# Performance work log

Measured on AMD Instinct MI355X. Metric: run time of the kernel, lower is better.

## Reference

```python
import jax, jax.numpy as jnp
import numpy as np

B, N, C, H = 8, 1024, 768, 12
D = C // H          # head_dim = 64
M = 2 * D           # rand_feat_dim = 128
SCALE = D ** -0.5
EPS = 1e-12         # F.normalize eps


def _feature_map(z, rand_matrix):
    # z: [B,H,N,D] already multiplied by sqrt(scale); proj: [H,D,M]
    logits = jnp.einsum('bhnd,hdm->bhnm', z, rand_matrix)
    sqnorm = 0.5 * jnp.sum(z * z, axis=-1, keepdims=True)
    return jnp.exp(logits - sqnorm) * (M ** -0.5)


def setup_inputs() -> dict:
    key = jax.random.key(0)
    k1, k2, k3, k4, k5 = jax.random.split(key, 5)
    x = jax.random.normal(k1, (B, N, C), dtype=jnp.float32)
    qkv_w = jax.random.normal(k2, (3 * C, C), dtype=jnp.float32) * 0.02
    proj_w = jax.random.normal(k3, (C, C), dtype=jnp.float32) * 0.02
    proj_b = jax.random.normal(k4, (C,), dtype=jnp.float32) * 0.02
    rand_matrix = jax.random.normal(k5, (H, D, M), dtype=jnp.float32)
    return {"x": x, "qkv_w": qkv_w, "proj_w": proj_w, "proj_b": proj_b,
            "rand_matrix": rand_matrix}


def reference(x, qkv_w, proj_w, proj_b, rand_matrix):
    b, n, c = x.shape
    # qkv projection (torch Linear, no bias): [B,N,3C] -> [3,B,H,N,D]
    qkv = (x @ qkv_w.T).reshape(b, n, 3, H, D).transpose(2, 0, 3, 1, 4)
    q, k, v = qkv[0], qkv[1], qkv[2]
    sq = SCALE ** 0.5
    qf = _feature_map(q * sq, rand_matrix)   # [B,H,N,M]
    kf = _feature_map(k * sq, rand_matrix)   # [B,H,N,M]
    attn = jnp.einsum('bhnm,bhkm->bhnk', qf, kf)          # explicit O(N^2)
    denom = jnp.maximum(jnp.sum(jnp.abs(attn), axis=-1, keepdims=True), EPS)
    attn = attn / denom                                   # L1 normalize
    out = jnp.einsum('bhnk,bhkd->bhnd', attn, v)          # [B,H,N,D]
    out = out.transpose(0, 2, 1, 3).reshape(b, n, c)
    return out @ proj_w.T + proj_b
```

## Files before the change

### kernel.cpp

```cpp
#include <hip/hip_runtime.h>
#include <hip/hip_bf16.h>

#define PB 8
#define PN 1024
#define PC 768
#define PH 12
#define PD 64
#define PM 128
#define SQ 0.35355339059327373f
#define MSCALE 0.08838834764831843f

typedef _Float16 f16;
typedef f16 f16x8 __attribute__((ext_vector_type(8)));
typedef f16 f16x4 __attribute__((ext_vector_type(4)));
typedef float f32x4 __attribute__((ext_vector_type(4)));

__global__ __launch_bounds__(192) void conv_hi(const float* __restrict__ src,
                                               f16* __restrict__ dst, int cols) {
    const int r = blockIdx.x;
    const int c = threadIdx.x * 4;
    float4 v = *(const float4*)&src[(size_t)r * cols + c];
    f16x4 hi;
    hi.x = (f16)v.x; hi.y = (f16)v.y; hi.z = (f16)v.z; hi.w = (f16)v.w;
    *(f16x4*)&dst[(size_t)r * cols + c] = hi;
}

__global__ __launch_bounds__(256) void conv_rt(const float* __restrict__ rm,
                                               f16* __restrict__ Rt) {
    const int h = blockIdx.x;
    for (int e = threadIdx.x; e < PD * PM; e += 256) {
        int m = e >> 6, d = e & 63;
        Rt[(size_t)h * PD * PM + e] = (f16)rm[(size_t)h * PD * PM + d * PM + m];
    }
}

__global__ __launch_bounds__(256) void gemm_qkv(
        const f16* __restrict__ A,
        const f16* __restrict__ Bm,
        f16* __restrict__ zq, f16* __restrict__ zk, f16* __restrict__ vh,
        float* __restrict__ sqq, float* __restrict__ sqk)
{
    __shared__ f16 As[128 * 32];
    __shared__ f16 Bs[128 * 32];
    const int t = threadIdx.x;
    const int wave = t >> 6, lane = t & 63;
    const int wm = wave >> 1, wn = wave & 1;
    const int bi = blockIdx.y * 128, bj = blockIdx.x * 128;

    f32x4 acc[4][4] = {};

    const int srow16 = lane >> 2;
    const int schunk = ((lane & 3) ^ ((lane >> 3) & 3)) * 8;
    const f16* Ap = A + (size_t)(bi + wave * 32 + srow16) * PC + schunk;
    f16* AsB = &As[wave * 32 * 32];
    const f16* Bp = Bm + (size_t)(bj + wave * 32 + srow16) * PC + schunk;
    f16* BsB = &Bs[wave * 32 * 32];

    for (int kt = 0; kt < 24; ++kt) {
        const int k0 = kt * 32;
        __syncthreads();
        __builtin_amdgcn_global_load_lds(
            (const __attribute__((address_space(1))) void*)(Ap + k0),
            (__attribute__((address_space(3))) void*)(AsB), 16, 0, 0);
        __builtin_amdgcn_global_load_lds(
            (const __attribute__((address_space(1))) void*)(Ap + k0 + (size_t)16 * PC),
            (__attribute__((address_space(3))) void*)(AsB + 16 * 32), 16, 0, 0);
        __builtin_amdgcn_global_load_lds(
            (const __attribute__((address_space(1))) void*)(Bp + k0),
            (__attribute__((address_space(3))) void*)(BsB), 16, 0, 0);
        __builtin_amdgcn_global_load_lds(
            (const __attribute__((address_space(1))) void*)(Bp + k0 + (size_t)16 * PC),
            (__attribute__((address_space(3))) void*)(BsB + 16 * 32), 16, 0, 0);
        __syncthreads();

        f16x8 af[4], bf[4];
        #pragma unroll
        for (int i = 0; i < 4; ++i) {
            const int r = wm * 64 + i * 16 + (lane & 15);
            const int p = (lane >> 4) ^ ((r >> 1) & 3);
            af[i] = *(const f16x8*)&As[r * 32 + p * 8];
        }
        #pragma unroll
        for (int j = 0; j < 4; ++j) {
            const int r = wn * 64 + j * 16 + (lane & 15);
            const int p = (lane >> 4) ^ ((r >> 1) & 3);
            bf[j] = *(const f16x8*)&Bs[r * 32 + p * 8];
        }
        #pragma unroll
        for (int i = 0; i < 4; ++i)
            #pragma unroll
            for (int j = 0; j < 4; ++j)
                acc[i][j] = __builtin_amdgcn_mfma_f32_16x16x32_f16(af[i], bf[j], acc[i][j], 0, 0, 0);
    }

    const int quad = lane >> 4, cc = lane & 15;
    const int colbase = bj + wn * 64;
    const int b = bi >> 10;
    if (colbase < 1536) {
        const int which = colbase >= 768;
        const int h = (colbase - which * 768) >> 6;
        f16* zdst = which ? zk : zq;
        float* sdst = which ? sqk : sqq;
        const size_t bh = (size_t)(b * PH + h);
        #pragma unroll
        for (int i = 0; i < 4; ++i) {
            const int row0 = bi + wm * 64 + i * 16 + quad * 4;
            #pragma unroll
            for (int r = 0; r < 4; ++r) {
                const int n = (row0 + r) & 1023;
                f16 zh[4]; float psq = 0.f;
                #pragma unroll
                for (int j = 0; j < 4; ++j) {
                    zh[j] = (f16)(acc[i][j][r] * SQ);
                    float zf = (float)zh[j];
                    psq += zf * zf;
                }
                psq += __shfl_xor(psq, 1, 64);
                psq += __shfl_xor(psq, 2, 64);
                psq += __shfl_xor(psq, 4, 64);
                psq += __shfl_xor(psq, 8, 64);
                if (cc == 0) sdst[(bh << 10) + n] = 0.5f * psq;
                f16* zp = zdst + (((bh << 10) + n) << 6);
                #pragma unroll
                for (int j = 0; j < 4; ++j) zp[j * 16 + cc] = zh[j];
            }
        }
    } else {
        const int h = (colbase - 1536) >> 6;
        const size_t bh = (size_t)(b * PH + h);
        #pragma unroll
        for (int i = 0; i < 4; ++i) {
            const int row0 = bi + wm * 64 + i * 16 + quad * 4;
            #pragma unroll
            for (int r = 0; r < 4; ++r) {
                const int n = (row0 + r) & 1023;
                f16* vp = vh + (((bh << 10) + n) << 6);
                #pragma unroll
                for (int j = 0; j < 4; ++j) vp[j * 16 + cc] = (f16)acc[i][j][r];
            }
        }
    }
}

__global__ __launch_bounds__(256) void feat_kv(
        const f16* __restrict__ zk, const f16* __restrict__ Rt,
        const float* __restrict__ sqk, const f16* __restrict__ vh,
        float* __restrict__ kvp, float* __restrict__ sbufp)
{
    __shared__ __align__(16) char smem[52224];
    f16* As = (f16*)smem;
    f16* Bs = (f16*)(smem + 8192);
    f16* Pt = (f16*)smem;
    f16* vT = (f16*)(smem + 34816);
    __shared__ float sqs[128];

    const int t = threadIdx.x;
    const int wave = t >> 6, lane = t & 63;
    const int wm = wave >> 1, wn = wave & 1;
    const int nt = blockIdx.x, bh = blockIdx.y;
    const int h = bh % PH;

    const f16* A = zk + (((size_t)bh << 10) + nt * 128) * 64;
    const f16* Bm = Rt + (size_t)h * (PM * PD);

    if (t < 128) sqs[t] = sqk[((size_t)bh << 10) + nt * 128 + t];

    f32x4 acc[4][4] = {};
    const int srow16 = lane >> 2;
    const int schunk = ((lane & 3) ^ ((lane >> 3) & 3)) * 8;
    const f16* Ap = A + (size_t)(wave * 32 + srow16) * 64 + schunk;
    f16* AsB = &As[wave * 32 * 32];
    const f16* Bp = Bm + (size_t)(wave * 32 + srow16) * 64 + schunk;
    f16* BsB = &Bs[wave * 32 * 32];

    #pragma unroll
    for (int kt = 0; kt < 2; ++kt) {
        const int k0 = kt * 32;
        __syncthreads();
        __builtin_amdgcn_global_load_lds(
            (const __attribute__((address_space(1))) void*)(Ap + k0),
            (__attribute__((address_space(3))) void*)(AsB), 16, 0, 0);
        __builtin_amdgcn_global_load_lds(
            (const __attribute__((address_space(1))) void*)(Ap + k0 + (size_t)16 * 64),
            (__attribute__((address_space(3))) void*)(AsB + 16 * 32), 16, 0, 0);
        __builtin_amdgcn_global_load_lds(
            (const __attribute__((address_space(1))) void*)(Bp + k0),
            (__attribute__((address_space(3))) void*)(BsB), 16, 0, 0);
        __builtin_amdgcn_global_load_lds(
            (const __attribute__((address_space(1))) void*)(Bp + k0 + (size_t)16 * 64),
            (__attribute__((address_space(3))) void*)(BsB + 16 * 32), 16, 0, 0);
        __syncthreads();

        f16x8 af[4], bf[4];
        #pragma unroll
        for (int i = 0; i < 4; ++i) {
            const int r = wm * 64 + i * 16 + (lane & 15);
            const int p = (lane >> 4) ^ ((r >> 1) & 3);
            af[i] = *(const f16x8*)&As[r * 32 + p * 8];
        }
        #pragma unroll
        for (int j = 0; j < 4; ++j) {
            const int r = wn * 64 + j * 16 + (lane & 15);
            const int p = (lane >> 4) ^ ((r >> 1) & 3);
            bf[j] = *(const f16x8*)&Bs[r * 32 + p * 8];
        }
        #pragma unroll
        for (int i = 0; i < 4; ++i)
            #pragma unroll
            for (int j = 0; j < 4; ++j)
                acc[i][j] = __builtin_amdgcn_mfma_f32_16x16x32_f16(af[i], bf[j], acc[i][j], 0, 0, 0);
    }

    const int quad = lane >> 4, cc = lane & 15;
    __syncthreads();

    #pragma unroll
    for (int i = 0; i < 4; ++i) {
        #pragma unroll
        for (int j = 0; j < 4; ++j) {
            const int col = wn * 64 + j * 16 + cc;
            #pragma unroll
            for (int r = 0; r < 4; ++r) {
                const int rl = wm * 64 + i * 16 + quad * 4 + r;
                Pt[col * 136 + rl] = (f16)(__expf(acc[i][j][r] - sqs[rl]) * MSCALE);
            }
        }
    }
    {
        const int vn = t >> 1;
        const int vhf = (t & 1) * 32;
        const f16* vbase = vh + (((size_t)bh << 10) + nt * 128 + vn) * 64 + vhf;
        #pragma unroll
        for (int k = 0; k < 4; ++k) {
            f16x8 vv = *(const f16x8*)&vbase[k * 8];
            #pragma unroll
            for (int e = 0; e < 8; ++e)
                vT[(vhf + k * 8 + e) * 136 + vn] = vv[e];
        }
    }
    __syncthreads();

    f32x4 acc2[4][2] = {};
    #pragma unroll
    for (int kt = 0; kt < 4; ++kt) {
        const int kb = kt * 32 + (lane >> 4) * 8;
        f16x8 af2[4], bf2[2];
        #pragma unroll
        for (int i = 0; i < 4; ++i)
            af2[i] = *(const f16x8*)&Pt[(wm * 64 + i * 16 + (lane & 15)) * 136 + kb];
        #pragma unroll
        for (int j = 0; j < 2; ++j)
            bf2[j] = *(const f16x8*)&vT[(wn * 32 + j * 16 + (lane & 15)) * 136 + kb];
        #pragma unroll
        for (int i = 0; i < 4; ++i)
            #pragma unroll
            for (int j = 0; j < 2; ++j)
                acc2[i][j] = __builtin_amdgcn_mfma_f32_16x16x32_f16(af2[i], bf2[j], acc2[i][j], 0, 0, 0);
    }

    float* kvo = kvp + (size_t)(nt * 96 + bh) * 8192;
    #pragma unroll
    for (int i = 0; i < 4; ++i) {
        #pragma unroll
        for (int j = 0; j < 2; ++j) {
            const int d = wn * 32 + j * 16 + cc;
            #pragma unroll
            for (int r = 0; r < 4; ++r) {
                const int m = wm * 64 + i * 16 + quad * 4 + r;
                kvo[m * 64 + d] = acc2[i][j][r];
            }
        }
    }
    {
        const int sm = t >> 1, shf = (t & 1) * 64;
        float sp = 0.f;
        #pragma unroll
        for (int k = 0; k < 8; ++k) {
            f16x8 pv = *(const f16x8*)&Pt[sm * 136 + shf + k * 8];
            #pragma unroll
            for (int e = 0; e < 8; ++e) sp += (float)pv[e];
        }
        sp += __shfl_xor(sp, 1, 64);
        if ((t & 1) == 0) sbufp[(size_t)(nt * 96 + bh) * 128 + sm] = sp;
    }
}

__global__ __launch_bounds__(256) void kv_reduce(
        const float* __restrict__ kvp, const float* __restrict__ sbufp,
        float* __restrict__ kv, float* __restrict__ s)
{
    const int idx = blockIdx.x * 256 + threadIdx.x;
    float a = 0.f;
    #pragma unroll
    for (int c = 0; c < 8; ++c) a += kvp[(size_t)c * 786432 + idx];
    kv[idx] = a;
    if (idx < 96 * PM) {
        float sa = 0.f;
        #pragma unroll
        for (int c = 0; c < 8; ++c) sa += sbufp[(size_t)c * 96 * PM + idx];
        s[idx] = sa;
    }
}

__global__ __launch_bounds__(256) void feat_apply(
        const f16* __restrict__ zq, const f16* __restrict__ Rt,
        const float* __restrict__ sqq, const float* __restrict__ kvf,
        const float* __restrict__ sf, f16* __restrict__ ohA)
{
    __shared__ __align__(16) char smem[52224];
    f16* As = (f16*)smem;
    f16* Bs = (f16*)(smem + 8192);
    f16* Pn = (f16*)smem;
    f16* kvT = (f16*)(smem + 34816);
    __shared__ float sqs[128], ssm[128], dns[128];

    const int t = threadIdx.x;
    const int wave = t >> 6, lane = t & 63;
    const int wm = wave >> 1, wn = wave & 1;
    const int nt = blockIdx.x, bh = blockIdx.y;
    const int b = bh / PH, h = bh % PH;

    const f16* A = zq + (((size_t)bh << 10) + nt * 128) * 64;
    const f16* Bm = Rt + (size_t)h * (PM * PD);

    if (t < 128) {
        sqs[t] = sqq[((size_t)bh << 10) + nt * 128 + t];
        ssm[t] = sf[(size_t)bh * 128 + t];
    }

    f32x4 acc[4][4] = {};
    const int srow16 = lane >> 2;
    const int schunk = ((lane & 3) ^ ((lane >> 3) & 3)) * 8;
    const f16* Ap = A + (size_t)(wave * 32 + srow16) * 64 + schunk;
    f16* AsB = &As[wave * 32 * 32];
    const f16* Bp = Bm + (size_t)(wave * 32 + srow16) * 64 + schunk;
    f16* BsB = &Bs[wave * 32 * 32];

    #pragma unroll
    for (int kt = 0; kt < 2; ++kt) {
        const int k0 = kt * 32;
        __syncthreads();
        __builtin_amdgcn_global_load_lds(
            (const __attribute__((address_space(1))) void*)(Ap + k0),
            (__attribute__((address_space(3))) void*)(AsB), 16, 0, 0);
        __builtin_amdgcn_global_load_lds(
            (const __attribute__((address_space(1))) void*)(Ap + k0 + (size_t)16 * 64),
            (__attribute__((address_space(3))) void*)(AsB + 16 * 32), 16, 0, 0);
        __builtin_amdgcn_global_load_lds(
            (const __attribute__((address_space(1))) void*)(Bp + k0),
            (__attribute__((address_space(3))) void*)(BsB), 16, 0, 0);
        __builtin_amdgcn_global_load_lds(
            (const __attribute__((address_space(1))) void*)(Bp + k0 + (size_t)16 * 64),
            (__attribute__((address_space(3))) void*)(BsB + 16 * 32), 16, 0, 0);
        __syncthreads();

        f16x8 af[4], bf[4];
        #pragma unroll
        for (int i = 0; i < 4; ++i) {
            const int r = wm * 64 + i * 16 + (lane & 15);
            const int p = (lane >> 4) ^ ((r >> 1) & 3);
            af[i] = *(const f16x8*)&As[r * 32 + p * 8];
        }
        #pragma unroll
        for (int j = 0; j < 4; ++j) {
            const int r = wn * 64 + j * 16 + (lane & 15);
            const int p = (lane >> 4) ^ ((r >> 1) & 3);
            bf[j] = *(const f16x8*)&Bs[r * 32 + p * 8];
        }
        #pragma unroll
        for (int i = 0; i < 4; ++i)
            #pragma unroll
            for (int j = 0; j < 4; ++j)
                acc[i][j] = __builtin_amdgcn_mfma_f32_16x16x32_f16(af[i], bf[j], acc[i][j], 0, 0, 0);
    }

    const int quad = lane >> 4, cc = lane & 15;
    __syncthreads();

    #pragma unroll
    for (int i = 0; i < 4; ++i) {
        #pragma unroll
        for (int j = 0; j < 4; ++j) {
            const int col = wn * 64 + j * 16 + cc;
            #pragma unroll
            for (int r = 0; r < 4; ++r) {
                const int rl = wm * 64 + i * 16 + quad * 4 + r;
                Pn[rl * 136 + col] = (f16)(__expf(acc[i][j][r] - sqs[rl]) * MSCALE);
            }
        }
    }
    {
        const int m = t >> 1;
        const int dh2 = (t & 1) * 32;
        const float* kvb = kvf + ((size_t)bh * 128 + m) * 64 + dh2;
        #pragma unroll
        for (int k = 0; k < 8; ++k) {
            float4 k4 = *(const float4*)&kvb[k * 4];
            kvT[(dh2 + k * 4 + 0) * 136 + m] = (f16)k4.x;
            kvT[(dh2 + k * 4 + 1) * 136 + m] = (f16)k4.y;
            kvT[(dh2 + k * 4 + 2) * 136 + m] = (f16)k4.z;
            kvT[(dh2 + k * 4 + 3) * 136 + m] = (f16)k4.w;
        }
    }
    __syncthreads();

    {
        const int n = t >> 1, mh = (t & 1) * 64;
        float p = 0.f;
        #pragma unroll
        for (int k = 0; k < 8; ++k) {
            f16x8 pv = *(const f16x8*)&Pn[n * 136 + mh + k * 8];
            #pragma unroll
            for (int e = 0; e < 8; ++e)
                p += (float)pv[e] * ssm[mh + k * 8 + e];
        }
        p += __shfl_xor(p, 1, 64);
        if ((t & 1) == 0) dns[n] = (p < 1e-12f) ? 1e-12f : p;
    }
    __syncthreads();

    f32x4 acc3[4][2] = {};
    #pragma unroll
    for (int kt = 0; kt < 4; ++kt) {
        const int kb = kt * 32 + (lane >> 4) * 8;
        f16x8 af3[4], bf3[2];
        #pragma unroll
        for (int i = 0; i < 4; ++i)
            af3[i] = *(const f16x8*)&Pn[(wm * 64 + i * 16 + (lane & 15)) * 136 + kb];
        #pragma unroll
        for (int j = 0; j < 2; ++j)
            bf3[j] = *(const f16x8*)&kvT[(wn * 32 + j * 16 + (lane & 15)) * 136 + kb];
        #pragma unroll
        for (int i = 0; i < 4; ++i)
            #pragma unroll
            for (int j = 0; j < 2; ++j)
                acc3[i][j] = __builtin_amdgcn_mfma_f32_16x16x32_f16(af3[i], bf3[j], acc3[i][j], 0, 0, 0);
    }

    f16* ob = ohA + ((size_t)(b * PN) + nt * 128) * PC + h * PD;
    #pragma unroll
    for (int i = 0; i < 4; ++i) {
        #pragma unroll
        for (int j = 0; j < 2; ++j) {
            const int d = wn * 32 + j * 16 + cc;
            #pragma unroll
            for (int r = 0; r < 4; ++r) {
                const int n = wm * 64 + i * 16 + quad * 4 + r;
                ob[(size_t)n * PC + d] = (f16)(acc3[i][j][r] / dns[n]);
            }
        }
    }
}

template<int BN>
__global__ __launch_bounds__(256) void gemm_mfma(
        const f16* __restrict__ A, int lda,
        const f16* __restrict__ Bm, int ldb,
        float* __restrict__ Cm, int ldc, int Kp,
        const float* __restrict__ bias)
{
    constexpr int JT = BN / 32;
    __shared__ f16 As[128 * 32];
    __shared__ f16 Bs[BN * 32];
    const int t = threadIdx.x;
    const int wave = t >> 6, lane = t & 63;
    const int wm = wave >> 1, wn = wave & 1;
    const int bi = blockIdx.y * 128, bj = blockIdx.x * BN;

    f32x4 acc[4][JT] = {};

    const int srow16 = lane >> 2;
    const int schunk = ((lane & 3) ^ ((lane >> 3) & 3)) * 8;
    const f16* Ap = A + (size_t)(bi + wave * 32 + srow16) * lda + schunk;
    f16* AsB = &As[wave * 32 * 32];
    const int brow0 = (BN == 128) ? wave * 32 : wave * 16;
    const f16* Bp = Bm + (size_t)(bj + brow0 + srow16) * ldb + schunk;
    f16* BsB = &Bs[brow0 * 32];

    const int nK = Kp / 32;
    for (int kt = 0; kt < nK; ++kt) {
        const int k0 = kt * 32;
        __syncthreads();
        __builtin_amdgcn_global_load_lds(
            (const __attribute__((address_space(1))) void*)(Ap + k0),
            (__attribute__((address_space(3))) void*)(AsB), 16, 0, 0);
        __builtin_amdgcn_global_load_lds(
            (const __attribute__((address_space(1))) void*)(Ap + k0 + (size_t)16 * lda),
            (__attribute__((address_space(3))) void*)(AsB + 16 * 32), 16, 0, 0);
        __builtin_amdgcn_global_load_lds(
            (const __attribute__((address_space(1))) void*)(Bp + k0),
            (__attribute__((address_space(3))) void*)(BsB), 16, 0, 0);
        if (BN == 128)
            __builtin_amdgcn_global_load_lds(
                (const __attribute__((address_space(1))) void*)(Bp + k0 + (size_t)16 * ldb),
                (__attribute__((address_space(3))) void*)(BsB + 16 * 32), 16, 0, 0);
        __syncthreads();

        f16x8 af[4], bf[JT];
        #pragma unroll
        for (int i = 0; i < 4; ++i) {
            const int r = wm * 64 + i * 16 + (lane & 15);
            const int p = (lane >> 4) ^ ((r >> 1) & 3);
            af[i] = *(const f16x8*)&As[r * 32 + p * 8];
        }
        #pragma unroll
        for (int j = 0; j < JT; ++j) {
            const int r = wn * (BN / 2) + j * 16 + (lane & 15);
            const int p = (lane >> 4) ^ ((r >> 1) & 3);
            bf[j] = *(const f16x8*)&Bs[r * 32 + p * 8];
        }
        #pragma unroll
        for (int i = 0; i < 4; ++i)
            #pragma unroll
            for (int j = 0; j < JT; ++j)
                acc[i][j] = __builtin_amdgcn_mfma_f32_16x16x32_f16(af[i], bf[j], acc[i][j], 0, 0, 0);
    }

    const int cr = (lane >> 4) * 4, cc = lane & 15;
    #pragma unroll
    for (int i = 0; i < 4; ++i) {
        const int row = bi + wm * 64 + i * 16 + cr;
        #pragma unroll
        for (int j = 0; j < JT; ++j) {
            const int col = bj + wn * (BN / 2) + j * 16 + cc;
            const float bv = bias ? bias[col] : 0.f;
            #pragma unroll
            for (int r = 0; r < 4; ++r)
                Cm[(size_t)(row + r) * ldc + col] = acc[i][j][r] + bv;
        }
    }
}

extern "C" void kernel_launch(void* const* d_in, const int* in_sizes, int n_in,
                              void* d_out, int out_size, void* d_ws, size_t ws_size,
                              hipStream_t stream) {
    const float* x      = (const float*)d_in[0];
    const float* qkv_w  = (const float*)d_in[1];
    const float* proj_w = (const float*)d_in[2];
    const float* proj_b = (const float*)d_in[3];
    const float* rm     = (const float*)d_in[4];
    float* out = (float*)d_out;

    char* ws = (char*)d_ws;
    f16*   Ax   = (f16*)(ws);
    f16*   Bqk  = (f16*)(ws + 12582912);
    f16*   Bp   = (f16*)(ws + 16121856);
    f16*   Rt   = (f16*)(ws + 17301504);
    f16*   zq   = (f16*)(ws + 17498112);
    f16*   zk   = (f16*)(ws + 30081024);
    f16*   vh   = (f16*)(ws + 42663936);
    float* sqq  = (float*)(ws + 55246848);
    float* sqk  = (float*)(ws + 55640064);
    float* sbufp= (float*)(ws + 56033280);
    float* kvf  = (float*)(ws + 56426496);
    float* sf   = (float*)(ws + 59572224);
    f16*   ohA  = (f16*)(ws + 59621376);
    float* kvp = (float*)d_out;

    conv_hi<<<8192, 192, 0, stream>>>(x, Ax, PC);
    conv_hi<<<2304, 192, 0, stream>>>(qkv_w, Bqk, PC);
    conv_hi<<<768, 192, 0, stream>>>(proj_w, Bp, PC);
    conv_rt<<<PH, 256, 0, stream>>>(rm, Rt);

    gemm_qkv<<<dim3(18, 64), 256, 0, stream>>>(Ax, Bqk, zq, zk, vh, sqq, sqk);

    feat_kv<<<dim3(8, 96), 256, 0, stream>>>(zk, Rt, sqk, vh, kvp, sbufp);
    kv_reduce<<<3072, 256, 0, stream>>>(kvp, sbufp, kvf, sf);

    feat_apply<<<dim3(8, 96), 256, 0, stream>>>(zq, Rt, sqq, kvf, sf, ohA);

    gemm_mfma<64><<<dim3(12, 64), 256, 0, stream>>>(ohA, PC, Bp, PC,
                                                    out, PC, PC, proj_b);
}
```

Measured before the change: 202.3 us.

## Widen GEMM K-tile to 64 with 8-way swizzle and fuse conversion kernels

Doubles the K-depth of the shared-memory tiles in the QKV, feature and projection GEMMs from 32 to 64, using a new 8-chunk XOR swizzle. This halves the number of barrier pairs per K loop and loads each feature kernel's operands in a single pass. It also merges the four fp32-to-fp16 conversion launches into one kernel, saving launch overhead. The cost is twice the LDS per GEMM block, which may lower occupancy, and more complex swizzled addressing that must stay bank-conflict free.

Measured after the change: 189.5 us. 1.07x faster.

```diff
diff --git a/kernel.cpp b/kernel.cpp
--- a/kernel.cpp
+++ b/kernel.cpp
@@ -15,22 +15,32 @@
 typedef f16 f16x4 __attribute__((ext_vector_type(4)));
 typedef float f32x4 __attribute__((ext_vector_type(4)));
 
-__global__ __launch_bounds__(192) void conv_hi(const float* __restrict__ src,
-                                               f16* __restrict__ dst, int cols) {
-    const int r = blockIdx.x;
-    const int c = threadIdx.x * 4;
-    float4 v = *(const float4*)&src[(size_t)r * cols + c];
-    f16x4 hi;
-    hi.x = (f16)v.x; hi.y = (f16)v.y; hi.z = (f16)v.z; hi.w = (f16)v.w;
-    *(f16x4*)&dst[(size_t)r * cols + c] = hi;
-}
-
-__global__ __launch_bounds__(256) void conv_rt(const float* __restrict__ rm,
-                                               f16* __restrict__ Rt) {
-    const int h = blockIdx.x;
-    for (int e = threadIdx.x; e < PD * PM; e += 256) {
-        int m = e >> 6, d = e & 63;
-        Rt[(size_t)h * PD * PM + e] = (f16)rm[(size_t)h * PD * PM + d * PM + m];
+#define GLL(src, dst) __builtin_amdgcn_global_load_lds( \
+    (const __attribute__((address_space(1))) void*)(src), \
+    (__attribute__((address_space(3))) void*)(dst), 16, 0, 0)
+
+__global__ __launch_bounds__(192) void conv_all(
+        const float* __restrict__ x, const float* __restrict__ qkv_w,
+        const float* __restrict__ proj_w, const float* __restrict__ rm,
+        f16* __restrict__ Ax, f16* __restrict__ Bqk, f16* __restrict__ Bp,
+        f16* __restrict__ Rt)
+{
+    const int bid = blockIdx.x;
+    const int t = threadIdx.x;
+    if (bid < 11264) {
+        const float* src; f16* dst; int r;
+        if (bid < 8192)       { src = x;      dst = Ax;  r = bid; }
+        else if (bid < 10496) { src = qkv_w;  dst = Bqk; r = bid - 8192; }
+        else                  { src = proj_w; dst = Bp;  r = bid - 10496; }
+        const int c = t * 4;
+        float4 v = *(const float4*)&src[(size_t)r * PC + c];
+        f16x4 hv;
+        hv.x = (f16)v.x; hv.y = (f16)v.y; hv.z = (f16)v.z; hv.w = (f16)v.w;
+        *(f16x4*)&dst[(size_t)r * PC + c] = hv;
+    } else {
+        const int h = bid - 11264;
+        for (int e = t; e < PD * PM; e += 192)
+            Rt[(size_t)h * 8192 + e] = (f16)rm[(size_t)h * 8192 + (e & 63) * PM + (e >> 6)];
     }
 }
 
@@ -40,8 +50,8 @@
         f16* __restrict__ zq, f16* __restrict__ zk, f16* __restrict__ vh,
         float* __restrict__ sqq, float* __restrict__ sqk)
 {
-    __shared__ f16 As[128 * 32];
-    __shared__ f16 Bs[128 * 32];
+    __shared__ f16 As[128 * 64];
+    __shared__ f16 Bs[128 * 64];
     const int t = threadIdx.x;
     const int wave = t >> 6, lane = t & 63;
     const int wm = wave >> 1, wn = wave & 1;
@@ -49,48 +59,50 @@
 
     f32x4 acc[4][4] = {};
 
-    const int srow16 = lane >> 2;
-    const int schunk = ((lane & 3) ^ ((lane >> 3) & 3)) * 8;
-    const f16* Ap = A + (size_t)(bi + wave * 32 + srow16) * PC + schunk;
-    f16* AsB = &As[wave * 32 * 32];
-    const f16* Bp = Bm + (size_t)(bj + wave * 32 + srow16) * PC + schunk;
-    f16* BsB = &Bs[wave * 32 * 32];
-
-    for (int kt = 0; kt < 24; ++kt) {
-        const int k0 = kt * 32;
+    const int rowi = lane >> 3;
+    const int cb = (lane & 7) ^ ((lane >> 4) & 3);
+    const f16* ApE = A + (size_t)(bi + wave * 32 + rowi) * PC + cb * 8;
+    const f16* ApO = A + (size_t)(bi + wave * 32 + rowi) * PC + (cb ^ 4) * 8;
+    const f16* BpE = Bm + (size_t)(bj + wave * 32 + rowi) * PC + cb * 8;
+    const f16* BpO = Bm + (size_t)(bj + wave * 32 + rowi) * PC + (cb ^ 4) * 8;
+    f16* AsB = &As[wave * 32 * 64];
+    f16* BsB = &Bs[wave * 32 * 64];
+
+    const int q4 = lane >> 4;
+    for (int kt = 0; kt < 12; ++kt) {
+        const int k0 = kt * 64;
         __syncthreads();
-        __builtin_amdgcn_global_load_lds(
-            (const __attribute__((address_space(1))) void*)(Ap + k0),
-            (__attribute__((address_space(3))) void*)(AsB), 16, 0, 0);
-        __builtin_amdgcn_global_load_lds(
-            (const __attribute__((address_space(1))) void*)(Ap + k0 + (size_t)16 * PC),
-            (__attribute__((address_space(3))) void*)(AsB + 16 * 32), 16, 0, 0);
-        __builtin_amdgcn_global_load_lds(
-            (const __attribute__((address_space(1))) void*)(Bp + k0),
-            (__attribute__((address_space(3))) void*)(BsB), 16, 0, 0);
-        __builtin_amdgcn_global_load_lds(
-            (const __attribute__((address_space(1))) void*)(Bp + k0 + (size_t)16 * PC),
-            (__attribute__((address_space(3))) void*)(BsB + 16 * 32), 16, 0, 0);
+        GLL(ApE + k0,               AsB);
+        GLL(ApO + k0 + (size_t) 8 * PC, AsB + 8 * 64);
+        GLL(ApE + k0 + (size_t)16 * PC, AsB + 16 * 64);
+        GLL(ApO + k0 + (size_t)24 * PC, AsB + 24 * 64);
+        GLL(BpE + k0,               BsB);
+        GLL(BpO + k0 + (size_t) 8 * PC, BsB + 8 * 64);
+        GLL(BpE + k0 + (size_t)16 * PC, BsB + 16 * 64);
+        GLL(BpO + k0 + (size_t)24 * PC, BsB + 24 * 64);
         __syncthreads();
 
-        f16x8 af[4], bf[4];
-        #pragma unroll
-        for (int i = 0; i < 4; ++i) {
-            const int r = wm * 64 + i * 16 + (lane & 15);
-            const int p = (lane >> 4) ^ ((r >> 1) & 3);
-            af[i] = *(const f16x8*)&As[r * 32 + p * 8];
-        }
-        #pragma unroll
-        for (int j = 0; j < 4; ++j) {
-            const int r = wn * 64 + j * 16 + (lane & 15);
-            const int p = (lane >> 4) ^ ((r >> 1) & 3);
-            bf[j] = *(const f16x8*)&Bs[r * 32 + p * 8];
-        }
-        #pragma unroll
-        for (int i = 0; i < 4; ++i)
-            #pragma unroll
-            for (int j = 0; j < 4; ++j)
-                acc[i][j] = __builtin_amdgcn_mfma_f32_16x16x32_f16(af[i], bf[j], acc[i][j], 0, 0, 0);
+        #pragma unroll
+        for (int kh = 0; kh < 2; ++kh) {
+            f16x8 af[4], bf[4];
+            #pragma unroll
+            for (int i = 0; i < 4; ++i) {
+                const int r = wm * 64 + i * 16 + (lane & 15);
+                const int p = (kh * 4 + q4) ^ ((r >> 1) & 7);
+                af[i] = *(const f16x8*)&As[r * 64 + p * 8];
+            }
+            #pragma unroll
+            for (int j = 0; j < 4; ++j) {
+                const int r = wn * 64 + j * 16 + (lane & 15);
+                const int p = (kh * 4 + q4) ^ ((r >> 1) & 7);
+                bf[j] = *(const f16x8*)&Bs[r * 64 + p * 8];
+            }
+            #pragma unroll
+            for (int i = 0; i < 4; ++i)
+                #pragma unroll
+                for (int j = 0; j < 4; ++j)
+                    acc[i][j] = __builtin_amdgcn_mfma_f32_16x16x32_f16(af[i], bf[j], acc[i][j], 0, 0, 0);
+        }
     }
 
     const int quad = lane >> 4, cc = lane & 15;
@@ -149,7 +161,7 @@
 {
     __shared__ __align__(16) char smem[52224];
     f16* As = (f16*)smem;
-    f16* Bs = (f16*)(smem + 8192);
+    f16* Bs = (f16*)(smem + 16384);
     f16* Pt = (f16*)smem;
     f16* vT = (f16*)(smem + 34816);
     __shared__ float sqs[128];
@@ -165,44 +177,40 @@
 
     if (t < 128) sqs[t] = sqk[((size_t)bh << 10) + nt * 128 + t];
 
+    const int rowi = lane >> 3;
+    const int cb = (lane & 7) ^ ((lane >> 4) & 3);
+    const f16* ApE = A + (size_t)(wave * 32 + rowi) * 64 + cb * 8;
+    const f16* ApO = A + (size_t)(wave * 32 + rowi) * 64 + (cb ^ 4) * 8;
+    const f16* BpE = Bm + (size_t)(wave * 32 + rowi) * 64 + cb * 8;
+    const f16* BpO = Bm + (size_t)(wave * 32 + rowi) * 64 + (cb ^ 4) * 8;
+    f16* AsB = &As[wave * 32 * 64];
+    f16* BsB = &Bs[wave * 32 * 64];
+    GLL(ApE,            AsB);
+    GLL(ApO + 8 * 64,   AsB + 8 * 64);
+    GLL(ApE + 16 * 64,  AsB + 16 * 64);
+    GLL(ApO + 24 * 64,  AsB + 24 * 64);
+    GLL(BpE,            BsB);
+    GLL(BpO + 8 * 64,   BsB + 8 * 64);
+    GLL(BpE + 16 * 64,  BsB + 16 * 64);
+    GLL(BpO + 24 * 64,  BsB + 24 * 64);
+    __syncthreads();
+
+    const int q4 = lane >> 4;
     f32x4 acc[4][4] = {};
-    const int srow16 = lane >> 2;
-    const int schunk = ((lane & 3) ^ ((lane >> 3) & 3)) * 8;
-    const f16* Ap = A + (size_t)(wave * 32 + srow16) * 64 + schunk;
-    f16* AsB = &As[wave * 32 * 32];
-    const f16* Bp = Bm + (size_t)(wave * 32 + srow16) * 64 + schunk;
-    f16* BsB = &Bs[wave * 32 * 32];
-
-    #pragma unroll
-    for (int kt = 0; kt < 2; ++kt) {
-        const int k0 = kt * 32;
-        __syncthreads();
-        __builtin_amdgcn_global_load_lds(
-            (const __attribute__((address_space(1))) void*)(Ap + k0),
-            (__attribute__((address_space(3))) void*)(AsB), 16, 0, 0);
-        __builtin_amdgcn_global_load_lds(
-            (const __attribute__((address_space(1))) void*)(Ap + k0 + (size_t)16 * 64),
-            (__attribute__((address_space(3))) void*)(AsB + 16 * 32), 16, 0, 0);
-        __builtin_amdgcn_global_load_lds(
-            (const __attribute__((address_space(1))) void*)(Bp + k0),
-            (__attribute__((address_space(3))) void*)(BsB), 16, 0, 0);
-        __builtin_amdgcn_global_load_lds(
-            (const __attribute__((address_space(1))) void*)(Bp + k0 + (size_t)16 * 64),
-            (__attribute__((address_space(3))) void*)(BsB + 16 * 32), 16, 0, 0);
-        __syncthreads();
-
+    #pragma unroll
+    for (int kh = 0; kh < 2; ++kh) {
         f16x8 af[4], bf[4];
         #pragma unroll
         for (int i = 0; i < 4; ++i) {
             const int r = wm * 64 + i * 16 + (lane & 15);
-            const int p = (lane >> 4) ^ ((r >> 1) & 3);
-            af[i] = *(const f16x8*)&As[r * 32 + p * 8];
+            const int p = (kh * 4 + q4) ^ ((r >> 1) & 7);
+            af[i] = *(const f16x8*)&As[r * 64 + p * 8];
         }
         #pragma unroll
         for (int j = 0; j < 4; ++j) {
             const int r = wn * 64 + j * 16 + (lane & 15);
-            const int p = (lane >> 4) ^ ((r >> 1) & 3);
-            bf[j] = *(const f16x8*)&Bs[r * 32 + p * 8];
+            const int p = (kh * 4 + q4) ^ ((r >> 1) & 7);
+            bf[j] = *(const f16x8*)&Bs[r * 64 + p * 8];
         }
         #pragma unroll
         for (int i = 0; i < 4; ++i)
@@ -309,7 +317,7 @@
 {
     __shared__ __align__(16) char smem[52224];
     f16* As = (f16*)smem;
-    f16* Bs = (f16*)(smem + 8192);
+    f16* Bs = (f16*)(smem + 16384);
     f16* Pn = (f16*)smem;
     f16* kvT = (f16*)(smem + 34816);
     __shared__ float sqs[128], ssm[128], dns[128];
@@ -328,44 +336,40 @@
         ssm[t] = sf[(size_t)bh * 128 + t];
     }
 
+    const int rowi = lane >> 3;
+    const int cb = (lane & 7) ^ ((lane >> 4) & 3);
+    const f16* ApE = A + (size_t)(wave * 32 + rowi) * 64 + cb * 8;
+    const f16* ApO = A + (size_t)(wave * 32 + rowi) * 64 + (cb ^ 4) * 8;
+    const f16* BpE = Bm + (size_t)(wave * 32 + rowi) * 64 + cb * 8;
+    const f16* BpO = Bm + (size_t)(wave * 32 + rowi) * 64 + (cb ^ 4) * 8;
+    f16* AsB = &As[wave * 32 * 64];
+    f16* BsB = &Bs[wave * 32 * 64];
+    GLL(ApE,            AsB);
+    GLL(ApO + 8 * 64,   AsB + 8 * 64);
+    GLL(ApE + 16 * 64,  AsB + 16 * 64);
+    GLL(ApO + 24 * 64,  AsB + 24 * 64);
+    GLL(BpE,            BsB);
+    GLL(BpO + 8 * 64,   BsB + 8 * 64);
+    GLL(BpE + 16 * 64,  BsB + 16 * 64);
+    GLL(BpO + 24 * 64,  BsB + 24 * 64);
+    __syncthreads();
+
+    const int q4 = lane >> 4;
     f32x4 acc[4][4] = {};
-    const int srow16 = lane >> 2;
-    const int schunk = ((lane & 3) ^ ((lane >> 3) & 3)) * 8;
-    const f16* Ap = A + (size_t)(wave * 32 + srow16) * 64 + schunk;
-    f16* AsB = &As[wave * 32 * 32];
-    const f16* Bp = Bm + (size_t)(wave * 32 + srow16) * 64 + schunk;
-    f16* BsB = &Bs[wave * 32 * 32];
-
-    #pragma unroll
-    for (int kt = 0; kt < 2; ++kt) {
-        const int k0 = kt * 32;
-        __syncthreads();
-        __builtin_amdgcn_global_load_lds(
-            (const __attribute__((address_space(1))) void*)(Ap + k0),
-            (__attribute__((address_space(3))) void*)(AsB), 16, 0, 0);
-        __builtin_amdgcn_global_load_lds(
-            (const __attribute__((address_space(1))) void*)(Ap + k0 + (size_t)16 * 64),
-            (__attribute__((address_space(3))) void*)(AsB + 16 * 32), 16, 0, 0);
-        __builtin_amdgcn_global_load_lds(
-            (const __attribute__((address_space(1))) void*)(Bp + k0),
-            (__attribute__((address_space(3))) void*)(BsB), 16, 0, 0);
-        __builtin_amdgcn_global_load_lds(
-            (const __attribute__((address_space(1))) void*)(Bp + k0 + (size_t)16 * 64),
-            (__attribute__((address_space(3))) void*)(BsB + 16 * 32), 16, 0, 0);
-        __syncthreads();
-
+    #pragma unroll
+    for (int kh = 0; kh < 2; ++kh) {
         f16x8 af[4], bf[4];
         #pragma unroll
         for (int i = 0; i < 4; ++i) {
             const int r = wm * 64 + i * 16 + (lane & 15);
-            const int p = (lane >> 4) ^ ((r >> 1) & 3);
-            af[i] = *(const f16x8*)&As[r * 32 + p * 8];
+            const int p = (kh * 4 + q4) ^ ((r >> 1) & 7);
+            af[i] = *(const f16x8*)&As[r * 64 + p * 8];
         }
         #pragma unroll
         for (int j = 0; j < 4; ++j) {
             const int r = wn * 64 + j * 16 + (lane & 15);
-            const int p = (lane >> 4) ^ ((r >> 1) & 3);
-            bf[j] = *(const f16x8*)&Bs[r * 32 + p * 8];
+            const int p = (kh * 4 + q4) ^ ((r >> 1) & 7);
+            bf[j] = *(const f16x8*)&Bs[r * 64 + p * 8];
         }
         #pragma unroll
         for (int i = 0; i < 4; ++i)
@@ -452,68 +456,62 @@
     }
 }
 
-template<int BN>
-__global__ __launch_bounds__(256) void gemm_mfma(
-        const f16* __restrict__ A, int lda,
-        const f16* __restrict__ Bm, int ldb,
-        float* __restrict__ Cm, int ldc, int Kp,
-        const float* __restrict__ bias)
+__global__ __launch_bounds__(256) void gemm_proj(
+        const f16* __restrict__ A,
+        const f16* __restrict__ Bm,
+        float* __restrict__ Cm, const float* __restrict__ bias)
 {
-    constexpr int JT = BN / 32;
-    __shared__ f16 As[128 * 32];
-    __shared__ f16 Bs[BN * 32];
+    __shared__ f16 As[128 * 64];
+    __shared__ f16 Bs[64 * 64];
     const int t = threadIdx.x;
     const int wave = t >> 6, lane = t & 63;
     const int wm = wave >> 1, wn = wave & 1;
-    const int bi = blockIdx.y * 128, bj = blockIdx.x * BN;
-
-    f32x4 acc[4][JT] = {};
-
-    const int srow16 = lane >> 2;
-    const int schunk = ((lane & 3) ^ ((lane >> 3) & 3)) * 8;
-    const f16* Ap = A + (size_t)(bi + wave * 32 + srow16) * lda + schunk;
-    f16* AsB = &As[wave * 32 * 32];
-    const int brow0 = (BN == 128) ? wave * 32 : wave * 16;
-    const f16* Bp = Bm + (size_t)(bj + brow0 + srow16) * ldb + schunk;
-    f16* BsB = &Bs[brow0 * 32];
-
-    const int nK = Kp / 32;
-    for (int kt = 0; kt < nK; ++kt) {
-        const int k0 = kt * 32;
+    const int bi = blockIdx.y * 128, bj = blockIdx.x * 64;
+
+    f32x4 acc[4][2] = {};
+
+    const int rowi = lane >> 3;
+    const int cb = (lane & 7) ^ ((lane >> 4) & 3);
+    const f16* ApE = A + (size_t)(bi + wave * 32 + rowi) * PC + cb * 8;
+    const f16* ApO = A + (size_t)(bi + wave * 32 + rowi) * PC + (cb ^ 4) * 8;
+    const f16* BpE = Bm + (size_t)(bj + wave * 16 + rowi) * PC + cb * 8;
+    const f16* BpO = Bm + (size_t)(bj + wave * 16 + rowi) * PC + (cb ^ 4) * 8;
+    f16* AsB = &As[wave * 32 * 64];
+    f16* BsB = &Bs[wave * 16 * 64];
+
+    const int q4 = lane >> 4;
+    for (int kt = 0; kt < 12; ++kt) {
+        const int k0 = kt * 64;
         __syncthreads();
-        __builtin_amdgcn_global_load_lds(
-            (const __attribute__((address_space(1))) void*)(Ap + k0),
-            (__attribute__((address_space(3))) void*)(AsB), 16, 0, 0);
-        __builtin_amdgcn_global_load_lds(
-            (const __attribute__((address_space(1))) void*)(Ap + k0 + (size_t)16 * lda),
-            (__attribute__((address_space(3))) void*)(AsB + 16 * 32), 16, 0, 0);
-        __builtin_amdgcn_global_load_lds(
-            (const __attribute__((address_space(1))) void*)(Bp + k0),
-            (__attribute__((address_space(3))) void*)(BsB), 16, 0, 0);
-        if (BN == 128)
-            __builtin_amdgcn_global_load_lds(
-                (const __attribute__((address_space(1))) void*)(Bp + k0 + (size_t)16 * ldb),
-                (__attribute__((address_space(3))) void*)(BsB + 16 * 32), 16, 0, 0);
+        GLL(ApE + k0,               AsB);
+        GLL(ApO + k0 + (size_t) 8 * PC, AsB + 8 * 64);
+        GLL(ApE + k0 + (size_t)16 * PC, AsB + 16 * 64);
+        GLL(ApO + k0 + (size_t)24 * PC, AsB + 24 * 64);
+        GLL(BpE + k0,               BsB);
+        GLL(BpO + k0 + (size_t) 8 * PC, BsB + 8 * 64);
         __syncthreads();
 
-        f16x8 af[4], bf[JT];
-        #pragma unroll
-        for (int i = 0; i < 4; ++i) {
-            const int r = wm * 64 + i * 16 + (lane & 15);
-            const int p = (lane >> 4) ^ ((r >> 1) & 3);
-            af[i] = *(const f16x8*)&As[r * 32 + p * 8];
-        }
-        #pragma unroll
-        for (int j = 0; j < JT; ++j) {
-            const int r = wn * (BN / 2) + j * 16 + (lane & 15);
-            const int p = (lane >> 4) ^ ((r >> 1) & 3);
-            bf[j] = *(const f16x8*)&Bs[r * 32 + p * 8];
-        }
-        #pragma unroll
-        for (int i = 0; i < 4; ++i)
-            #pragma unroll
-            for (int j = 0; j < JT; ++j)
-                acc[i][j] = __builtin_amdgcn_mfma_f32_16x16x32_f16(af[i], bf[j], acc[i][j], 0, 0, 0);
+        #pragma unroll
+        for (int kh = 0; kh < 2; ++kh) {
+            f16x8 af[4], bf[2];
+            #pragma unroll
+            for (int i = 0; i < 4; ++i) {
+                const int r = wm * 64 + i * 16 + (lane & 15);
+                const int p = (kh * 4 + q4) ^ ((r >> 1) & 7);
+                af[i] = *(const f16x8*)&As[r * 64 + p * 8];
+            }
+            #pragma unroll
+            for (int j = 0; j < 2; ++j) {
+                const int r = wn * 32 + j * 16 + (lane & 15);
+                const int p = (kh * 4 + q4) ^ ((r >> 1) & 7);
+                bf[j] = *(const f16x8*)&Bs[r * 64 + p * 8];
+            }
+            #pragma unroll
+            for (int i = 0; i < 4; ++i)
+                #pragma unroll
+                for (int j = 0; j < 2; ++j)
+                    acc[i][j] = __builtin_amdgcn_mfma_f32_16x16x32_f16(af[i], bf[j], acc[i][j], 0, 0, 0);
+        }
     }
 
     const int cr = (lane >> 4) * 4, cc = lane & 15;
@@ -521,12 +519,12 @@
     for (int i = 0; i < 4; ++i) {
         const int row = bi + wm * 64 + i * 16 + cr;
         #pragma unroll
-        for (int j = 0; j < JT; ++j) {
-            const int col = bj + wn * (BN / 2) + j * 16 + cc;
-            const float bv = bias ? bias[col] : 0.f;
+        for (int j = 0; j < 2; ++j) {
+            const int col = bj + wn * 32 + j * 16 + cc;
+            const float bv = bias[col];
             #pragma unroll
             for (int r = 0; r < 4; ++r)
-                Cm[(size_t)(row + r) * ldc + col] = acc[i][j][r] + bv;
+                Cm[(size_t)(row + r) * PC + col] = acc[i][j][r] + bv;
         }
     }
 }
@@ -557,10 +555,7 @@
     f16*   ohA  = (f16*)(ws + 59621376);
     float* kvp = (float*)d_out;
 
-    conv_hi<<<8192, 192, 0, stream>>>(x, Ax, PC);
-    conv_hi<<<2304, 192, 0, stream>>>(qkv_w, Bqk, PC);
-    conv_hi<<<768, 192, 0, stream>>>(proj_w, Bp, PC);
-    conv_rt<<<PH, 256, 0, stream>>>(rm, Rt);
+    conv_all<<<11276, 192, 0, stream>>>(x, qkv_w, proj_w, rm, Ax, Bqk, Bp, Rt);
 
     gemm_qkv<<<dim3(18, 64), 256, 0, stream>>>(Ax, Bqk, zq, zk, vh, sqq, sqk);
 
@@ -569,6 +564,5 @@
 
     feat_apply<<<dim3(8, 96), 256, 0, stream>>>(zq, Rt, sqq, kvf, sf, ohA);
 
-    gemm_mfma<64><<<dim3(12, 64), 256, 0, stream>>>(ohA, PC, Bp, PC,
-                                                    out, PC, PC, proj_b);
-}
+    gemm_proj<<<dim3(12, 64), 256, 0, stream>>>(ohA, Bp, out, proj_b);
+}
```
